# Kernel optimization log

Hardware: AMD Instinct MI355X
Metric: run time of the kernel (lower is better)

The kernel has to match this reference:

```python
import jax, jax.numpy as jnp
import numpy as np

V, E, H, L = 10000, 512, 1024, 2
B, S = 64, 128
STEPS = 143  # hard-coded decode loop length in the original module


def setup_inputs() -> dict:
    key = jax.random.key(0)
    ks = jax.random.split(key, 12)
    s = 0.05  # keep recurrent dynamics stable
    d = dict(
        x=jax.random.randint(ks[0], (B, S), 0, V),
        emb=jax.random.normal(ks[1], (V, E), jnp.float32) * s,
        Wih0=jax.random.normal(ks[2], (4 * H, E), jnp.float32) * s,
        Whh0=jax.random.normal(ks[3], (4 * H, H), jnp.float32) * s,
        bih0=jax.random.normal(ks[4], (4 * H,), jnp.float32) * s,
        bhh0=jax.random.normal(ks[5], (4 * H,), jnp.float32) * s,
        Wih1=jax.random.normal(ks[6], (4 * H, H), jnp.float32) * s,
        Whh1=jax.random.normal(ks[7], (4 * H, H), jnp.float32) * s,
        bih1=jax.random.normal(ks[8], (4 * H,), jnp.float32) * s,
        bhh1=jax.random.normal(ks[9], (4 * H,), jnp.float32) * s,
        Wfc=jax.random.normal(ks[10], (V, H), jnp.float32) * s,
        bfc=jax.random.normal(ks[11], (V,), jnp.float32) * s,
    )
    return d


def _cell(x, h, c, Wih, Whh, bih, bhh):
    # PyTorch LSTM gate order: i, f, g, o
    gates = x @ Wih.T + h @ Whh.T + (bih + bhh)
    i, f, g, o = jnp.split(gates, 4, axis=-1)
    c_new = jax.nn.sigmoid(f) * c + jax.nn.sigmoid(i) * jnp.tanh(g)
    h_new = jax.nn.sigmoid(o) * jnp.tanh(c_new)
    return h_new, c_new


def _stack_step(layers, inp, h, c):
    hs, cs = [], []
    for l, (Wih, Whh, bih, bhh) in enumerate(layers):
        hn, cn = _cell(inp, h[l], c[l], Wih, Whh, bih, bhh)
        hs.append(hn)
        cs.append(cn)
        inp = hn
    return jnp.stack(hs), jnp.stack(cs), inp


def reference(x, emb, Wih0, Whh0, bih0, bhh0, Wih1, Whh1, bih1, bhh1, Wfc, bfc):
    layers = [(Wih0, Whh0, bih0, bhh0), (Wih1, Whh1, bih1, bhh1)]
    b = x.shape[0]
    hd = Whh0.shape[1]
    embedded = emb[x]                      # [B, S, E]
    h0 = jnp.zeros((len(layers), b, hd), embedded.dtype)
    c0 = jnp.zeros_like(h0)

    def enc_step(carry, xt):               # xt: [B, E]
        h, c = carry
        h, c, out = _stack_step(layers, xt, h, c)
        return (h, c), out

    (h, c), outs = jax.lax.scan(enc_step, (h0, c0), jnp.swapaxes(embedded, 0, 1))
    last = outs[-1]                         # [B, H]
    first_logits = last @ Wfc.T + bfc       # [B, V]
    # Faithful quirk: argmax over the raw hidden state (dim H), used as token ids.
    tok0 = jnp.argmax(last, axis=-1)

    def dec_step(carry, _):
        h, c, tok = carry
        inp = emb[tok]                      # [B, E]
        h, c, out = _stack_step(layers, inp, h, c)
        logits = out @ Wfc.T + bfc          # [B, V]
        tok = jnp.argmax(logits, axis=-1)
        return (h, c, tok), logits

    _, dec_logits = jax.lax.scan(dec_step, (h, c, tok0), None, length=STEPS)
    # predictions: [B, 1 + STEPS, V]
    preds = jnp.concatenate([first_logits[:, None, :], jnp.swapaxes(dec_logits, 0, 1)], axis=1)
    return preds
```

## Files before the change

### kernel.cpp

```cpp
#include <hip/hip_runtime.h>
#include <cfloat>
#include <cmath>

namespace {

constexpr int Bn = 64;
constexpr int Sn = 128;
constexpr int En = 512;
constexpr int Hn = 1024;
constexpr int Vn = 10000;
constexpr int Tn = 144;
constexpr int DEC = 143;
constexpr int ENC_CHUNK = 16;

__device__ __forceinline__ double sigd(double x) { return 1.0 / (1.0 + exp(-x)); }

__global__ __launch_bounds__(256) void init_state(double* __restrict__ ws) {
    const size_t i = (size_t)blockIdx.x * blockDim.x + threadIdx.x;
    ws[i] = 0.0;
}

__global__ __launch_bounds__(256) void gather_enc(
    const int* __restrict__ x, const float* __restrict__ emb,
    float* __restrict__ xt, const int t0)
{
    const int b  = (int)blockIdx.x & 63;
    const int ti = (int)blockIdx.x >> 6;
    const int token = x[b * Sn + t0 + ti];
    const float* __restrict__ er = emb + (size_t)token * En;
    float* __restrict__ xo = xt + (size_t)ti * En * 64;
    for (int k = (int)threadIdx.x; k < En; k += 256)
        xo[(size_t)k * 64 + b] = er[k];
}

template<typename XT, int KX>
__global__ __launch_bounds__(256) void cell_kernel(
    const XT*     __restrict__ xt,
    const double* __restrict__ hin,
    double*       __restrict__ hout,
    double*       __restrict__ cst,
    const float*  __restrict__ Wih,
    const float*  __restrict__ Whh,
    const float*  __restrict__ bih,
    const float*  __restrict__ bhh)
{
    __shared__ double part[4][4][64];
    const int tid = (int)threadIdx.x;
    const int b = tid & 63;
    const int w = tid >> 6;
    const int j = (int)blockIdx.x;

    double a0 = 0.0, a1 = 0.0, a2 = 0.0, a3 = 0.0;

    {
        constexpr int C = KX / 4;
        const int k0 = w * C;
        const float4* __restrict__ r0 = (const float4*)(Wih + (size_t)(0 * Hn + j) * KX + k0);
        const float4* __restrict__ r1 = (const float4*)(Wih + (size_t)(1 * Hn + j) * KX + k0);
        const float4* __restrict__ r2 = (const float4*)(Wih + (size_t)(2 * Hn + j) * KX + k0);
        const float4* __restrict__ r3 = (const float4*)(Wih + (size_t)(3 * Hn + j) * KX + k0);
        const XT* __restrict__ xp = xt + (size_t)k0 * 64 + b;
        #pragma unroll 2
        for (int i = 0; i < C / 4; ++i) {
            const float4 w0 = r0[i], w1 = r1[i], w2 = r2[i], w3 = r3[i];
            const double x0 = (double)xp[(size_t)(4 * i + 0) * 64];
            const double x1 = (double)xp[(size_t)(4 * i + 1) * 64];
            const double x2 = (double)xp[(size_t)(4 * i + 2) * 64];
            const double x3 = (double)xp[(size_t)(4 * i + 3) * 64];
            a0 = fma(x0, (double)w0.x, a0); a0 = fma(x1, (double)w0.y, a0);
            a0 = fma(x2, (double)w0.z, a0); a0 = fma(x3, (double)w0.w, a0);
            a1 = fma(x0, (double)w1.x, a1); a1 = fma(x1, (double)w1.y, a1);
            a1 = fma(x2, (double)w1.z, a1); a1 = fma(x3, (double)w1.w, a1);
            a2 = fma(x0, (double)w2.x, a2); a2 = fma(x1, (double)w2.y, a2);
            a2 = fma(x2, (double)w2.z, a2); a2 = fma(x3, (double)w2.w, a2);
            a3 = fma(x0, (double)w3.x, a3); a3 = fma(x1, (double)w3.y, a3);
            a3 = fma(x2, (double)w3.z, a3); a3 = fma(x3, (double)w3.w, a3);
        }
    }
    {
        constexpr int C = Hn / 4;
        const int k0 = w * C;
        const float4* __restrict__ r0 = (const float4*)(Whh + (size_t)(0 * Hn + j) * Hn + k0);
        const float4* __restrict__ r1 = (const float4*)(Whh + (size_t)(1 * Hn + j) * Hn + k0);
        const float4* __restrict__ r2 = (const float4*)(Whh + (size_t)(2 * Hn + j) * Hn + k0);
        const float4* __restrict__ r3 = (const float4*)(Whh + (size_t)(3 * Hn + j) * Hn + k0);
        const double* __restrict__ hp = hin + (size_t)k0 * 64 + b;
        #pragma unroll 2
        for (int i = 0; i < C / 4; ++i) {
            const float4 w0 = r0[i], w1 = r1[i], w2 = r2[i], w3 = r3[i];
            const double x0 = hp[(size_t)(4 * i + 0) * 64];
            const double x1 = hp[(size_t)(4 * i + 1) * 64];
            const double x2 = hp[(size_t)(4 * i + 2) * 64];
            const double x3 = hp[(size_t)(4 * i + 3) * 64];
            a0 = fma(x0, (double)w0.x, a0); a0 = fma(x1, (double)w0.y, a0);
            a0 = fma(x2, (double)w0.z, a0); a0 = fma(x3, (double)w0.w, a0);
            a1 = fma(x0, (double)w1.x, a1); a1 = fma(x1, (double)w1.y, a1);
            a1 = fma(x2, (double)w1.z, a1); a1 = fma(x3, (double)w1.w, a1);
            a2 = fma(x0, (double)w2.x, a2); a2 = fma(x1, (double)w2.y, a2);
            a2 = fma(x2, (double)w2.z, a2); a2 = fma(x3, (double)w2.w, a2);
            a3 = fma(x0, (double)w3.x, a3); a3 = fma(x1, (double)w3.y, a3);
            a3 = fma(x2, (double)w3.z, a3); a3 = fma(x3, (double)w3.w, a3);
        }
    }

    part[w][0][b] = a0; part[w][1][b] = a1; part[w][2][b] = a2; part[w][3][b] = a3;
    __syncthreads();

    if (tid < 64) {
        const int bb = tid;
        const double ai = (double)bih[0 * Hn + j] + (double)bhh[0 * Hn + j]
                        + part[0][0][bb] + part[1][0][bb] + part[2][0][bb] + part[3][0][bb];
        const double af = (double)bih[1 * Hn + j] + (double)bhh[1 * Hn + j]
                        + part[0][1][bb] + part[1][1][bb] + part[2][1][bb] + part[3][1][bb];
        const double ag = (double)bih[2 * Hn + j] + (double)bhh[2 * Hn + j]
                        + part[0][2][bb] + part[1][2][bb] + part[2][2][bb] + part[3][2][bb];
        const double ao = (double)bih[3 * Hn + j] + (double)bhh[3 * Hn + j]
                        + part[0][3][bb] + part[1][3][bb] + part[2][3][bb] + part[3][3][bb];
        const double ig = sigd(ai);
        const double fg = sigd(af);
        const double gg = tanh(ag);
        const double og = sigd(ao);
        const size_t idx = (size_t)j * 64 + bb;
        const double cn = fg * cst[idx] + ig * gg;
        cst[idx] = cn;
        hout[idx] = og * tanh(cn);
    }
}

__global__ __launch_bounds__(256) void logits_kernel(
    const double* __restrict__ h,
    const float*  __restrict__ Wfc,
    const float*  __restrict__ bfc,
    float*        __restrict__ outf)
{
    __shared__ double part[4][4][64];
    const int tid = (int)threadIdx.x;
    const int b = tid & 63;
    const int w = tid >> 6;
    const int v0 = (int)blockIdx.x * 4;
    double a0 = 0.0, a1 = 0.0, a2 = 0.0, a3 = 0.0;
    const int k0 = w * (Hn / 4);
    const float4* __restrict__ r0 = (const float4*)(Wfc + (size_t)(v0 + 0) * Hn + k0);
    const float4* __restrict__ r1 = (const float4*)(Wfc + (size_t)(v0 + 1) * Hn + k0);
    const float4* __restrict__ r2 = (const float4*)(Wfc + (size_t)(v0 + 2) * Hn + k0);
    const float4* __restrict__ r3 = (const float4*)(Wfc + (size_t)(v0 + 3) * Hn + k0);
    const double* __restrict__ hp = h + (size_t)k0 * 64 + b;
    #pragma unroll 2
    for (int i = 0; i < Hn / 16; ++i) {
        const float4 w0 = r0[i], w1 = r1[i], w2 = r2[i], w3 = r3[i];
        const double x0 = hp[(size_t)(4 * i + 0) * 64];
        const double x1 = hp[(size_t)(4 * i + 1) * 64];
        const double x2 = hp[(size_t)(4 * i + 2) * 64];
        const double x3 = hp[(size_t)(4 * i + 3) * 64];
        a0 = fma(x0, (double)w0.x, a0); a0 = fma(x1, (double)w0.y, a0);
        a0 = fma(x2, (double)w0.z, a0); a0 = fma(x3, (double)w0.w, a0);
        a1 = fma(x0, (double)w1.x, a1); a1 = fma(x1, (double)w1.y, a1);
        a1 = fma(x2, (double)w1.z, a1); a1 = fma(x3, (double)w1.w, a1);
        a2 = fma(x0, (double)w2.x, a2); a2 = fma(x1, (double)w2.y, a2);
        a2 = fma(x2, (double)w2.z, a2); a2 = fma(x3, (double)w2.w, a2);
        a3 = fma(x0, (double)w3.x, a3); a3 = fma(x1, (double)w3.y, a3);
        a3 = fma(x2, (double)w3.z, a3); a3 = fma(x3, (double)w3.w, a3);
    }
    part[w][0][b] = a0; part[w][1][b] = a1; part[w][2][b] = a2; part[w][3][b] = a3;
    __syncthreads();
    const int vi = tid >> 6;
    const int bb = tid & 63;
    const double s = (double)bfc[v0 + vi]
                   + part[0][vi][bb] + part[1][vi][bb] + part[2][vi][bb] + part[3][vi][bb];
    outf[(size_t)bb * ((size_t)Tn * Vn) + v0 + vi] = (float)s;
}

template<typename T>
__global__ __launch_bounds__(256) void argmax_gather(
    const T* __restrict__ vals, const int n, const int estride, const size_t bstride,
    const float* __restrict__ emb, float* __restrict__ xt)
{
    __shared__ double sv[256];
    __shared__ int si[256];
    __shared__ int stok;
    const int tid = (int)threadIdx.x;
    const int b = (int)blockIdx.x;
    const T* __restrict__ row = vals + (size_t)b * bstride;
    double best = -DBL_MAX;
    int bi = 0x7fffffff;
    for (int k = tid; k < n; k += 256) {
        const double v = (double)row[(size_t)k * estride];
        if (v > best) { best = v; bi = k; }
    }
    sv[tid] = best; si[tid] = bi;
    __syncthreads();
    for (int s = 128; s > 0; s >>= 1) {
        if (tid < s) {
            if (sv[tid + s] > sv[tid] || (sv[tid + s] == sv[tid] && si[tid + s] < si[tid])) {
                sv[tid] = sv[tid + s];
                si[tid] = si[tid + s];
            }
        }
        __syncthreads();
    }
    if (tid == 0) stok = si[0];
    __syncthreads();
    const float* __restrict__ er = emb + (size_t)stok * En;
    for (int k = tid; k < En; k += 256)
        xt[(size_t)k * 64 + b] = er[k];
}

}

extern "C" void kernel_launch(void* const* d_in, const int* in_sizes, int n_in,
                              void* d_out, int out_size, void* d_ws, size_t ws_size,
                              hipStream_t stream)
{
    const int*   x    = (const int*)d_in[0];
    const float* emb  = (const float*)d_in[1];
    const float* Wih0 = (const float*)d_in[2];
    const float* Whh0 = (const float*)d_in[3];
    const float* bih0 = (const float*)d_in[4];
    const float* bhh0 = (const float*)d_in[5];
    const float* Wih1 = (const float*)d_in[6];
    const float* Whh1 = (const float*)d_in[7];
    const float* bih1 = (const float*)d_in[8];
    const float* bhh1 = (const float*)d_in[9];
    const float* Wfc  = (const float*)d_in[10];
    const float* bfc  = (const float*)d_in[11];
    float* out = (float*)d_out;

    double* ws = (double*)d_ws;
    const size_t BH = (size_t)Bn * Hn;
    double* h0 = ws;
    double* h1 = ws + 2 * BH;
    double* c0 = ws + 4 * BH;
    double* c1 = ws + 5 * BH;
    float*  xt = (float*)(ws + 6 * BH);

    init_state<<<1536, 256, 0, stream>>>(ws);

    int p = 0;
    for (int t0 = 0; t0 < Sn; t0 += ENC_CHUNK) {
        gather_enc<<<ENC_CHUNK * 64, 256, 0, stream>>>(x, emb, xt, t0);
        for (int ti = 0; ti < ENC_CHUNK; ++ti) {
            cell_kernel<float, En><<<Hn, 256, 0, stream>>>(
                xt + (size_t)ti * En * 64,
                h0 + (size_t)p * BH, h0 + (size_t)(1 - p) * BH, c0,
                Wih0, Whh0, bih0, bhh0);
            cell_kernel<double, Hn><<<Hn, 256, 0, stream>>>(
                h0 + (size_t)(1 - p) * BH,
                h1 + (size_t)p * BH, h1 + (size_t)(1 - p) * BH, c1,
                Wih1, Whh1, bih1, bhh1);
            p ^= 1;
        }
    }

    logits_kernel<<<2500, 256, 0, stream>>>(h1 + (size_t)p * BH, Wfc, bfc, out);
    argmax_gather<double><<<64, 256, 0, stream>>>(
        h1 + (size_t)p * BH, Hn, 64, 1, emb, xt);

    for (int s = 0; s < DEC; ++s) {
        cell_kernel<float, En><<<Hn, 256, 0, stream>>>(
            xt,
            h0 + (size_t)p * BH, h0 + (size_t)(1 - p) * BH, c0,
            Wih0, Whh0, bih0, bhh0);
        cell_kernel<double, Hn><<<Hn, 256, 0, stream>>>(
            h0 + (size_t)(1 - p) * BH,
            h1 + (size_t)p * BH, h1 + (size_t)(1 - p) * BH, c1,
            Wih1, Whh1, bih1, bhh1);
        p ^= 1;
        logits_kernel<<<2500, 256, 0, stream>>>(
            h1 + (size_t)p * BH, Wfc, bfc, out + (size_t)(1 + s) * Vn);
        if (s + 1 < DEC) {
            argmax_gather<float><<<64, 256, 0, stream>>>(
                out + (size_t)(1 + s) * Vn, Vn, 1, (size_t)Tn * Vn, emb, xt);
        }
    }

    (void)in_sizes; (void)n_in; (void)out_size; (void)ws_size;
}
```

Measured before the change: 80.62 ms.

## Register-tile four hidden units per block in LSTM cell and logits GEMVs

Each cell block now computes 4 hidden units (16 gate rows) with 512 threads splitting K eight ways. Each logits block computes 16 vocab rows. Every loaded activation value (h or x, in fp64) is reused across 16 weight rows instead of 4, which cuts redundant activation reads from global/L2 by 4x. The cost is many more accumulators and weight pointers per thread, which raises register pressure, and far fewer blocks (256 cell, 625 logits), which may reduce occupancy and latency hiding.

```diff
diff --git a/kernel.cpp b/kernel.cpp
--- a/kernel.cpp
+++ b/kernel.cpp
@@ -33,8 +33,44 @@
         xo[(size_t)k * 64 + b] = er[k];
 }
 
+template<typename XT, int K>
+__device__ __forceinline__ void gemv_part(
+    double (&acc)[4][4],
+    const XT* __restrict__ xcol,
+    const float* __restrict__ W,
+    const int j0, const int k0)
+{
+    const float4* r[4][4];
+    #pragma unroll
+    for (int jj = 0; jj < 4; ++jj)
+        #pragma unroll
+        for (int g = 0; g < 4; ++g)
+            r[jj][g] = (const float4*)(W + ((size_t)g * Hn + (j0 + jj)) * K + k0);
+    const XT* __restrict__ xp = xcol + (size_t)k0 * 64;
+    constexpr int C = K / 8;
+    #pragma unroll 2
+    for (int i = 0; i < C / 4; ++i) {
+        const double x0 = (double)xp[(size_t)(4 * i + 0) * 64];
+        const double x1 = (double)xp[(size_t)(4 * i + 1) * 64];
+        const double x2 = (double)xp[(size_t)(4 * i + 2) * 64];
+        const double x3 = (double)xp[(size_t)(4 * i + 3) * 64];
+        #pragma unroll
+        for (int jj = 0; jj < 4; ++jj)
+            #pragma unroll
+            for (int g = 0; g < 4; ++g) {
+                const float4 wv = r[jj][g][i];
+                double a = acc[jj][g];
+                a = fma(x0, (double)wv.x, a);
+                a = fma(x1, (double)wv.y, a);
+                a = fma(x2, (double)wv.z, a);
+                a = fma(x3, (double)wv.w, a);
+                acc[jj][g] = a;
+            }
+    }
+}
+
 template<typename XT, int KX>
-__global__ __launch_bounds__(256) void cell_kernel(
+__global__ __launch_bounds__(512, 2) void cell_kernel(
     const XT*     __restrict__ xt,
     const double* __restrict__ hin,
     double*       __restrict__ hout,
@@ -44,82 +80,40 @@
     const float*  __restrict__ bih,
     const float*  __restrict__ bhh)
 {
-    __shared__ double part[4][4][64];
+    __shared__ double part[8][16][64];
     const int tid = (int)threadIdx.x;
     const int b = tid & 63;
     const int w = tid >> 6;
-    const int j = (int)blockIdx.x;
-
-    double a0 = 0.0, a1 = 0.0, a2 = 0.0, a3 = 0.0;
-
-    {
-        constexpr int C = KX / 4;
-        const int k0 = w * C;
-        const float4* __restrict__ r0 = (const float4*)(Wih + (size_t)(0 * Hn + j) * KX + k0);
-        const float4* __restrict__ r1 = (const float4*)(Wih + (size_t)(1 * Hn + j) * KX + k0);
-        const float4* __restrict__ r2 = (const float4*)(Wih + (size_t)(2 * Hn + j) * KX + k0);
-        const float4* __restrict__ r3 = (const float4*)(Wih + (size_t)(3 * Hn + j) * KX + k0);
-        const XT* __restrict__ xp = xt + (size_t)k0 * 64 + b;
-        #pragma unroll 2
-        for (int i = 0; i < C / 4; ++i) {
-            const float4 w0 = r0[i], w1 = r1[i], w2 = r2[i], w3 = r3[i];
-            const double x0 = (double)xp[(size_t)(4 * i + 0) * 64];
-            const double x1 = (double)xp[(size_t)(4 * i + 1) * 64];
-            const double x2 = (double)xp[(size_t)(4 * i + 2) * 64];
-            const double x3 = (double)xp[(size_t)(4 * i + 3) * 64];
-            a0 = fma(x0, (double)w0.x, a0); a0 = fma(x1, (double)w0.y, a0);
-            a0 = fma(x2, (double)w0.z, a0); a0 = fma(x3, (double)w0.w, a0);
-            a1 = fma(x0, (double)w1.x, a1); a1 = fma(x1, (double)w1.y, a1);
-            a1 = fma(x2, (double)w1.z, a1); a1 = fma(x3, (double)w1.w, a1);
-            a2 = fma(x0, (double)w2.x, a2); a2 = fma(x1, (double)w2.y, a2);
-            a2 = fma(x2, (double)w2.z, a2); a2 = fma(x3, (double)w2.w, a2);
-            a3 = fma(x0, (double)w3.x, a3); a3 = fma(x1, (double)w3.y, a3);
-            a3 = fma(x2, (double)w3.z, a3); a3 = fma(x3, (double)w3.w, a3);
-        }
-    }
-    {
-        constexpr int C = Hn / 4;
-        const int k0 = w * C;
-        const float4* __restrict__ r0 = (const float4*)(Whh + (size_t)(0 * Hn + j) * Hn + k0);
-        const float4* __restrict__ r1 = (const float4*)(Whh + (size_t)(1 * Hn + j) * Hn + k0);
-        const float4* __restrict__ r2 = (const float4*)(Whh + (size_t)(2 * Hn + j) * Hn + k0);
-        const float4* __restrict__ r3 = (const float4*)(Whh + (size_t)(3 * Hn + j) * Hn + k0);
-        const double* __restrict__ hp = hin + (size_t)k0 * 64 + b;
-        #pragma unroll 2
-        for (int i = 0; i < C / 4; ++i) {
-            const float4 w0 = r0[i], w1 = r1[i], w2 = r2[i], w3 = r3[i];
-            const double x0 = hp[(size_t)(4 * i + 0) * 64];
-            const double x1 = hp[(size_t)(4 * i + 1) * 64];
-            const double x2 = hp[(size_t)(4 * i + 2) * 64];
-            const double x3 = hp[(size_t)(4 * i + 3) * 64];
-            a0 = fma(x0, (double)w0.x, a0); a0 = fma(x1, (double)w0.y, a0);
-            a0 = fma(x2, (double)w0.z, a0); a0 = fma(x3, (double)w0.w, a0);
-            a1 = fma(x0, (double)w1.x, a1); a1 = fma(x1, (double)w1.y, a1);
-            a1 = fma(x2, (double)w1.z, a1); a1 = fma(x3, (double)w1.w, a1);
-            a2 = fma(x0, (double)w2.x, a2); a2 = fma(x1, (double)w2.y, a2);
-            a2 = fma(x2, (double)w2.z, a2); a2 = fma(x3, (double)w2.w, a2);
-            a3 = fma(x0, (double)w3.x, a3); a3 = fma(x1, (double)w3.y, a3);
-            a3 = fma(x2, (double)w3.z, a3); a3 = fma(x3, (double)w3.w, a3);
-        }
-    }
-
-    part[w][0][b] = a0; part[w][1][b] = a1; part[w][2][b] = a2; part[w][3][b] = a3;
-    __syncthreads();
-
-    if (tid < 64) {
-        const int bb = tid;
-        const double ai = (double)bih[0 * Hn + j] + (double)bhh[0 * Hn + j]
-                        + part[0][0][bb] + part[1][0][bb] + part[2][0][bb] + part[3][0][bb];
-        const double af = (double)bih[1 * Hn + j] + (double)bhh[1 * Hn + j]
-                        + part[0][1][bb] + part[1][1][bb] + part[2][1][bb] + part[3][1][bb];
-        const double ag = (double)bih[2 * Hn + j] + (double)bhh[2 * Hn + j]
-                        + part[0][2][bb] + part[1][2][bb] + part[2][2][bb] + part[3][2][bb];
-        const double ao = (double)bih[3 * Hn + j] + (double)bhh[3 * Hn + j]
-                        + part[0][3][bb] + part[1][3][bb] + part[2][3][bb] + part[3][3][bb];
-        const double ig = sigd(ai);
-        const double fg = sigd(af);
-        const double gg = tanh(ag);
-        const double og = sigd(ao);
+    const int j0 = (int)blockIdx.x * 4;
+
+    double acc[4][4] = {};
+
+    gemv_part<XT, KX>(acc, xt + b, Wih, j0, w * (KX / 8));
+    gemv_part<double, Hn>(acc, hin + b, Whh, j0, w * (Hn / 8));
+
+    #pragma unroll
+    for (int jj = 0; jj < 4; ++jj)
+        #pragma unroll
+        for (int g = 0; g < 4; ++g)
+            part[w][jj * 4 + g][b] = acc[jj][g];
+    __syncthreads();
+
+    if (tid < 256) {
+        const int bb = tid & 63;
+        const int jj = tid >> 6;
+        const int j = j0 + jj;
+        double sg[4];
+        #pragma unroll
+        for (int g = 0; g < 4; ++g) {
+            double a = (double)bih[g * Hn + j] + (double)bhh[g * Hn + j];
+            #pragma unroll
+            for (int ww = 0; ww < 8; ++ww) a += part[ww][jj * 4 + g][bb];
+            sg[g] = a;
+        }
+        const double ig = sigd(sg[0]);
+        const double fg = sigd(sg[1]);
+        const double gg = tanh(sg[2]);
+        const double og = sigd(sg[3]);
         const size_t idx = (size_t)j * 64 + bb;
         const double cn = fg * cst[idx] + ig * gg;
         cst[idx] = cn;
@@ -127,47 +121,56 @@
     }
 }
 
-__global__ __launch_bounds__(256) void logits_kernel(
+__global__ __launch_bounds__(512, 2) void logits_kernel(
     const double* __restrict__ h,
     const float*  __restrict__ Wfc,
     const float*  __restrict__ bfc,
     float*        __restrict__ outf)
 {
-    __shared__ double part[4][4][64];
+    __shared__ double part[8][16][64];
     const int tid = (int)threadIdx.x;
     const int b = tid & 63;
     const int w = tid >> 6;
-    const int v0 = (int)blockIdx.x * 4;
-    double a0 = 0.0, a1 = 0.0, a2 = 0.0, a3 = 0.0;
-    const int k0 = w * (Hn / 4);
-    const float4* __restrict__ r0 = (const float4*)(Wfc + (size_t)(v0 + 0) * Hn + k0);
-    const float4* __restrict__ r1 = (const float4*)(Wfc + (size_t)(v0 + 1) * Hn + k0);
-    const float4* __restrict__ r2 = (const float4*)(Wfc + (size_t)(v0 + 2) * Hn + k0);
-    const float4* __restrict__ r3 = (const float4*)(Wfc + (size_t)(v0 + 3) * Hn + k0);
+    const int v0 = (int)blockIdx.x * 16;
+
+    double acc[16] = {};
+    const int k0 = w * (Hn / 8);
+    const float4* r[16];
+    #pragma unroll
+    for (int vv = 0; vv < 16; ++vv)
+        r[vv] = (const float4*)(Wfc + (size_t)(v0 + vv) * Hn + k0);
     const double* __restrict__ hp = h + (size_t)k0 * 64 + b;
     #pragma unroll 2
-    for (int i = 0; i < Hn / 16; ++i) {
-        const float4 w0 = r0[i], w1 = r1[i], w2 = r2[i], w3 = r3[i];
+    for (int i = 0; i < (Hn / 8) / 4; ++i) {
         const double x0 = hp[(size_t)(4 * i + 0) * 64];
         const double x1 = hp[(size_t)(4 * i + 1) * 64];
         const double x2 = hp[(size_t)(4 * i + 2) * 64];
         const double x3 = hp[(size_t)(4 * i + 3) * 64];
-        a0 = fma(x0, (double)w0.x, a0); a0 = fma(x1, (double)w0.y, a0);
-        a0 = fma(x2, (double)w0.z, a0); a0 = fma(x3, (double)w0.w, a0);
-        a1 = fma(x0, (double)w1.x, a1); a1 = fma(x1, (double)w1.y, a1);
-        a1 = fma(x2, (double)w1.z, a1); a1 = fma(x3, (double)w1.w, a1);
-        a2 = fma(x0, (double)w2.x, a2); a2 = fma(x1, (double)w2.y, a2);
-        a2 = fma(x2, (double)w2.z, a2); a2 = fma(x3, (double)w2.w, a2);
-        a3 = fma(x0, (double)w3.x, a3); a3 = fma(x1, (double)w3.y, a3);
-        a3 = fma(x2, (double)w3.z, a3); a3 = fma(x3, (double)w3.w, a3);
-    }
-    part[w][0][b] = a0; part[w][1][b] = a1; part[w][2][b] = a2; part[w][3][b] = a3;
-    __syncthreads();
-    const int vi = tid >> 6;
+        #pragma unroll
+        for (int vv = 0; vv < 16; ++vv) {
+            const float4 wv = r[vv][i];
+            double a = acc[vv];
+            a = fma(x0, (double)wv.x, a);
+            a = fma(x1, (double)wv.y, a);
+            a = fma(x2, (double)wv.z, a);
+            a = fma(x3, (double)wv.w, a);
+            acc[vv] = a;
+        }
+    }
+    #pragma unroll
+    for (int vv = 0; vv < 16; ++vv) part[w][vv][b] = acc[vv];
+    __syncthreads();
+
     const int bb = tid & 63;
-    const double s = (double)bfc[v0 + vi]
-                   + part[0][vi][bb] + part[1][vi][bb] + part[2][vi][bb] + part[3][vi][bb];
-    outf[(size_t)bb * ((size_t)Tn * Vn) + v0 + vi] = (float)s;
+    const int vh = tid >> 6;
+    #pragma unroll
+    for (int t2 = 0; t2 < 2; ++t2) {
+        const int vv = vh + t2 * 8;
+        double s = (double)bfc[v0 + vv];
+        #pragma unroll
+        for (int ww = 0; ww < 8; ++ww) s += part[ww][vv][bb];
+        outf[(size_t)bb * ((size_t)Tn * Vn) + v0 + vv] = (float)s;
+    }
 }
 
 template<typename T>
@@ -239,11 +242,11 @@
     for (int t0 = 0; t0 < Sn; t0 += ENC_CHUNK) {
         gather_enc<<<ENC_CHUNK * 64, 256, 0, stream>>>(x, emb, xt, t0);
         for (int ti = 0; ti < ENC_CHUNK; ++ti) {
-            cell_kernel<float, En><<<Hn, 256, 0, stream>>>(
+            cell_kernel<float, En><<<Hn / 4, 512, 0, stream>>>(
                 xt + (size_t)ti * En * 64,
                 h0 + (size_t)p * BH, h0 + (size_t)(1 - p) * BH, c0,
                 Wih0, Whh0, bih0, bhh0);
-            cell_kernel<double, Hn><<<Hn, 256, 0, stream>>>(
+            cell_kernel<double, Hn><<<Hn / 4, 512, 0, stream>>>(
                 h0 + (size_t)(1 - p) * BH,
                 h1 + (size_t)p * BH, h1 + (size_t)(1 - p) * BH, c1,
                 Wih1, Whh1, bih1, bhh1);
@@ -251,21 +254,21 @@
         }
     }
 
-    logits_kernel<<<2500, 256, 0, stream>>>(h1 + (size_t)p * BH, Wfc, bfc, out);
+    logits_kernel<<<Vn / 16, 512, 0, stream>>>(h1 + (size_t)p * BH, Wfc, bfc, out);
     argmax_gather<double><<<64, 256, 0, stream>>>(
         h1 + (size_t)p * BH, Hn, 64, 1, emb, xt);
 
     for (int s = 0; s < DEC; ++s) {
-        cell_kernel<float, En><<<Hn, 256, 0, stream>>>(
+        cell_kernel<float, En><<<Hn / 4, 512, 0, stream>>>(
             xt,
             h0 + (size_t)p * BH, h0 + (size_t)(1 - p) * BH, c0,
             Wih0, Whh0, bih0, bhh0);
-        cell_kernel<double, Hn><<<Hn, 256, 0, stream>>>(
+        cell_kernel<double, Hn><<<Hn / 4, 512, 0, stream>>>(
             h0 + (size_t)(1 - p) * BH,
             h1 + (size_t)p * BH, h1 + (size_t)(1 - p) * BH, c1,
             Wih1, Whh1, bih1, bhh1);
         p ^= 1;
-        logits_kernel<<<2500, 256, 0, stream>>>(
+        logits_kernel<<<Vn / 16, 512, 0, stream>>>(
             h1 + (size_t)p * BH, Wfc, bfc, out + (size_t)(1 + s) * Vn);
         if (s + 1 < DEC) {
             argmax_gather<float><<<64, 256, 0, stream>>>(
```

New measurement: 82.72 ms. +2.6%, slower.
